# Kernel optimization log

Measured on AMD Instinct MI355X. Metric: run time of the kernel, lower is better.

Reference implementation:

```python
import jax, jax.numpy as jnp
import numpy as np

N_NODES = 100000
N_EDGES = 1600000
IN_F = 128
HID = 16
NEG_SLOPE = 0.2


def setup_inputs() -> dict:
    key = jax.random.key(0)
    ks = jax.random.split(key, 12)
    x = jax.random.normal(ks[0], (N_NODES, IN_F), dtype=jnp.float32)
    edge_index = jax.random.randint(ks[1], (2, N_EDGES), 0, N_NODES, dtype=jnp.int32)
    s1 = 1.0 / np.sqrt(IN_F)
    s2 = 1.0 / np.sqrt(2 * HID)
    # layer 1: heads=2, out=16, concat -> 32
    W1 = jax.random.normal(ks[2], (IN_F, 2 * HID), dtype=jnp.float32) * s1
    a_src1 = jax.random.normal(ks[3], (2, HID), dtype=jnp.float32) * s2
    a_dst1 = jax.random.normal(ks[4], (2, HID), dtype=jnp.float32) * s2
    b1 = jnp.zeros((2 * HID,), dtype=jnp.float32)
    # layer 2: heads=1, out=1
    W2 = jax.random.normal(ks[5], (2 * HID, 1), dtype=jnp.float32) * s2
    a_src2 = jax.random.normal(ks[6], (1, 1), dtype=jnp.float32)
    a_dst2 = jax.random.normal(ks[7], (1, 1), dtype=jnp.float32)
    b2 = jnp.zeros((1,), dtype=jnp.float32)
    return {"x": x, "edge_index": edge_index, "W1": W1, "a_src1": a_src1,
            "a_dst1": a_dst1, "b1": b1, "W2": W2, "a_src2": a_src2,
            "a_dst2": a_dst2, "b2": b2}


def gat_conv(x, src, dst, W, a_src, a_dst, bias, heads, out_ch, concat):
    # PyG GATConv: linear proj, per-edge leaky-relu score, segment softmax over
    # incoming edges (dst), scatter-add aggregation. Self loops already in src/dst.
    n = x.shape[0]
    h = (x @ W).reshape(n, heads, out_ch)                      # [N,H,C]
    alpha_s = (h * a_src[None]).sum(-1)                        # [N,H]
    alpha_d = (h * a_dst[None]).sum(-1)                        # [N,H]
    e = jax.nn.leaky_relu(alpha_s[src] + alpha_d[dst], NEG_SLOPE)  # [E,H]
    m = jax.lax.stop_gradient(jax.ops.segment_max(e, dst, num_segments=n))
    ex = jnp.exp(e - m[dst])
    denom = jax.ops.segment_sum(ex, dst, num_segments=n)       # [N,H]
    alpha = ex / (denom[dst] + 1e-16)                          # [E,H]
    out = jax.ops.segment_sum(alpha[..., None] * h[src], dst, num_segments=n)  # [N,H,C]
    out = out.reshape(n, heads * out_ch) if concat else out.mean(axis=1)
    return out + bias


def reference(x, edge_index, W1, a_src1, a_dst1, b1, W2, a_src2, a_dst2, b2):
    n = x.shape[0]
    loop = jnp.arange(n, dtype=edge_index.dtype)
    src = jnp.concatenate([edge_index[0], loop])
    dst = jnp.concatenate([edge_index[1], loop])
    h = jax.nn.elu(gat_conv(x, src, dst, W1, a_src1, a_dst1, b1, 2, HID, True))
    out = gat_conv(h, src, dst, W2, a_src2, a_dst2, b2, 1, 1, False)
    return out
```

## Files before the change

kernel.cpp:

```cpp
#include <hip/hip_runtime.h>
#include <math.h>

#define IN_F 128
#define C1 32
#define NEG 0.2f
#define BSZ 128
#define CAP 2560
#define EPB 2048
#define TPW 2

typedef _Float16 h16;
typedef _Float16 h16x2 __attribute__((ext_vector_type(2)));
typedef _Float16 h16x4 __attribute__((ext_vector_type(4)));
typedef _Float16 h16x8 __attribute__((ext_vector_type(8)));
typedef float f32x4 __attribute__((ext_vector_type(4)));

__device__ __forceinline__ float leaky(float x) { return x >= 0.f ? x : NEG * x; }

__global__ __launch_bounds__(256)
void k_fat(const float* __restrict__ x, const float* __restrict__ W1,
           const float* __restrict__ a_s, const float* __restrict__ a_d,
           h16* __restrict__ h1h, float* __restrict__ as1,
           float* __restrict__ ad1, int N,
           const int* __restrict__ ei, int E, int ET, int nbk,
           int* __restrict__ bcnt, int* __restrict__ ebuf, int nproj) {
    __shared__ int smem[6144];
    int t = threadIdx.x;
    if ((int)blockIdx.x < nproj) {
        int wid = t >> 6, lane = t & 63;
        int q = lane >> 4, r = lane & 15;
        h16x8 Bf[2][4];
        #pragma unroll
        for (int ct = 0; ct < 2; ++ct)
            #pragma unroll
            for (int kc = 0; kc < 4; ++kc)
                #pragma unroll
                for (int j = 0; j < 8; ++j)
                    Bf[ct][kc][j] = (h16)W1[(kc * 32 + q * 8 + j) * C1 + ct * 16 + r];
        float a_s0 = a_s[r], a_s1v = a_s[16 + r];
        float a_d0 = a_d[r], a_d1v = a_d[16 + r];
        #pragma unroll
        for (int tt = 0; tt < TPW; ++tt) {
            int tile = (blockIdx.x * 4 + wid) * TPW + tt;
            int m0 = tile << 4;
            if (m0 >= N) break;
            int row = m0 + r; if (row >= N) row = N - 1;
            const float* xr = x + (size_t)row * IN_F + q * 8;
            f32x4 acc0 = {0.f, 0.f, 0.f, 0.f};
            f32x4 acc1 = {0.f, 0.f, 0.f, 0.f};
            #pragma unroll
            for (int kc = 0; kc < 4; ++kc) {
                float4 xa = *(const float4*)(xr + kc * 32);
                float4 xb = *(const float4*)(xr + kc * 32 + 4);
                h16x8 A;
                A[0] = (h16)xa.x; A[1] = (h16)xa.y; A[2] = (h16)xa.z; A[3] = (h16)xa.w;
                A[4] = (h16)xb.x; A[5] = (h16)xb.y; A[6] = (h16)xb.z; A[7] = (h16)xb.w;
                acc0 = __builtin_amdgcn_mfma_f32_16x16x32_f16(A, Bf[0][kc], acc0, 0, 0, 0);
                acc1 = __builtin_amdgcn_mfma_f32_16x16x32_f16(A, Bf[1][kc], acc1, 0, 0, 0);
            }
            #pragma unroll
            for (int reg = 0; reg < 4; ++reg) {
                int node = m0 + q * 4 + reg;
                bool vld = node < N;
                float h0 = acc0[reg], h1 = acc1[reg];
                if (vld) {
                    h1h[(size_t)node * C1 + r]      = (h16)h0;
                    h1h[(size_t)node * C1 + 16 + r] = (h16)h1;
                }
                float s0 = h0 * a_s0, s1 = h1 * a_s1v;
                float d0 = h0 * a_d0, d1 = h1 * a_d1v;
                s0 += __shfl_xor(s0, 1); s0 += __shfl_xor(s0, 2); s0 += __shfl_xor(s0, 4); s0 += __shfl_xor(s0, 8);
                s1 += __shfl_xor(s1, 1); s1 += __shfl_xor(s1, 2); s1 += __shfl_xor(s1, 4); s1 += __shfl_xor(s1, 8);
                d0 += __shfl_xor(d0, 1); d0 += __shfl_xor(d0, 2); d0 += __shfl_xor(d0, 4); d0 += __shfl_xor(d0, 8);
                d1 += __shfl_xor(d1, 1); d1 += __shfl_xor(d1, 2); d1 += __shfl_xor(d1, 4); d1 += __shfl_xor(d1, 8);
                if (vld && r == 0) {
                    *(float2*)&as1[node * 2] = make_float2(s0, s1);
                    *(float2*)&ad1[node * 2] = make_float2(d0, d1);
                }
            }
        }
    } else {
        int* hist = smem;
        int* lcur = hist + 1024;
        int2* ecache = (int2*)(lcur + 1024);
        int bid = blockIdx.x - nproj;
        hist[t] = 0; hist[t + 256] = 0; hist[t + 512] = 0; hist[t + 768] = 0;
        __syncthreads();
        int i0 = bid * EPB, i1 = min(ET, i0 + EPB);
        for (int i = i0 + t; i < i1; i += 256) {
            int s, d;
            if (i < E) { s = ei[i]; d = ei[E + i]; } else { s = d = i - E; }
            ecache[i - i0] = make_int2(s, d);
            atomicAdd(&hist[d >> 7], 1);
        }
        __syncthreads();
        for (int b = t; b < nbk; b += 256) {
            int h = hist[b];
            int base = h ? atomicAdd(&bcnt[b], h) : 0;
            lcur[b] = b * CAP + base;
        }
        __syncthreads();
        for (int i = i0 + t; i < i1; i += 256) {
            int2 e = ecache[i - i0];
            int bkt = e.y >> 7;
            int pos = atomicAdd(&lcur[bkt], 1);
            if (pos < (bkt + 1) * CAP)
                ebuf[pos] = (e.x << 7) | (e.y & 127);
        }
    }
}

__global__ __launch_bounds__(512)
void k_bagg(const int* __restrict__ bcnt, const int* __restrict__ ebuf,
            int N, int nbk, int ET,
            const float* __restrict__ as1, const float* __restrict__ ad1,
            const float* __restrict__ b1, const float* __restrict__ W2,
            const h16* __restrict__ h1h, int* __restrict__ off,
            int* __restrict__ csr1, float* __restrict__ p2) {
    __shared__ int2 elist[CAP];
    __shared__ int deg[BSZ], sst[BSZ], cur[BSZ];
    __shared__ float adl[BSZ * 2];
    __shared__ int red[8];
    int b = blockIdx.x, t = threadIdx.x;
    int cnt = min(bcnt[b], CAP);
    int ebase = b * CAP;
    int n0 = b * BSZ;
    int part = 0;
    for (int k = t; k < b; k += 512) part += min(bcnt[k], CAP);
    part += __shfl_xor(part, 1);  part += __shfl_xor(part, 2);
    part += __shfl_xor(part, 4);  part += __shfl_xor(part, 8);
    part += __shfl_xor(part, 16); part += __shfl_xor(part, 32);
    if ((t & 63) == 0) red[t >> 6] = part;
    if (t < BSZ) {
        deg[t] = 0;
        int n = n0 + t;
        float2 v = (n < N) ? ((const float2*)ad1)[n] : make_float2(0.f, 0.f);
        adl[t * 2] = v.x; adl[t * 2 + 1] = v.y;
    }
    __syncthreads();
    int fbase = red[0] + red[1] + red[2] + red[3] + red[4] + red[5] + red[6] + red[7];
    if (b == nbk - 1 && t == 0) off[N] = ET;
    for (int i = t; i < cnt; i += 512)
        atomicAdd(&deg[ebuf[ebase + i] & 127], 1);
    __syncthreads();
    int v = (t < BSZ) ? deg[t] : 0;
    __syncthreads();
    for (int o = 1; o < BSZ; o <<= 1) {
        int xv = (t >= o && t < BSZ) ? deg[t - o] : 0;
        __syncthreads();
        if (t < BSZ) deg[t] += xv;
        __syncthreads();
    }
    if (t < BSZ) {
        int excl = deg[t] - v;
        sst[t] = excl; cur[t] = excl;
        if (n0 + t < N) off[n0 + t] = fbase + excl;
    }
    __syncthreads();
    for (int i = t; i < cnt; i += 512) {
        int e = ebuf[ebase + i];
        int dl = e & 127, s = e >> 7;
        float2 asv = ((const float2*)as1)[s];
        float w0 = __expf(leaky(asv.x + adl[dl * 2 + 0]));
        float w1 = __expf(leaky(asv.y + adl[dl * 2 + 1]));
        h16x2 wp = { (h16)w0, (h16)w1 };
        int p = atomicAdd(&cur[dl], 1);
        int2 rec; rec.x = s; rec.y = *(int*)&wp;
        elist[p] = rec;
        csr1[fbase + p] = s;
    }
    __syncthreads();
    int l = t & 7, slot = t >> 3, c0 = l * 4, head = l >> 2;
    float b1l[4] = { b1[c0], b1[c0 + 1], b1[c0 + 2], b1[c0 + 3] };
    float w2l[4] = { W2[c0], W2[c0 + 1], W2[c0 + 2], W2[c0 + 3] };
    #pragma unroll
    for (int pass = 0; pass < 2; ++pass) {
        int dl = pass * 64 + slot;
        int node = n0 + dl;
        if (node >= N) break;
        int j0 = sst[dl], j1 = deg[dl];
        float den = 0.f, a0 = 0.f, a1 = 0.f, a2 = 0.f, a3 = 0.f;
        for (int j = j0; j < j1; j += 4) {
            #pragma unroll
            for (int k = 0; k < 4; ++k) {
                int jj = j + k;
                bool valid = jj < j1;
                jj = valid ? jj : j0;
                int2 e = elist[jj];
                int s = e.x;
                h16x2 wv = *(h16x2*)&e.y;
                float w = valid ? (float)(head ? wv.y : wv.x) : 0.f;
                h16x4 hv = *(const h16x4*)(h1h + ((size_t)s << 5) + c0);
                den += w;
                a0 = fmaf(w, (float)hv.x, a0);
                a1 = fmaf(w, (float)hv.y, a1);
                a2 = fmaf(w, (float)hv.z, a2);
                a3 = fmaf(w, (float)hv.w, a3);
            }
        }
        float inv = 1.f / (den + 1e-16f);
        float o, val = 0.f;
        o = a0 * inv + b1l[0]; o = o > 0.f ? o : expm1f(o); val = fmaf(o, w2l[0], val);
        o = a1 * inv + b1l[1]; o = o > 0.f ? o : expm1f(o); val = fmaf(o, w2l[1], val);
        o = a2 * inv + b1l[2]; o = o > 0.f ? o : expm1f(o); val = fmaf(o, w2l[2], val);
        o = a3 * inv + b1l[3]; o = o > 0.f ? o : expm1f(o); val = fmaf(o, w2l[3], val);
        val += __shfl_xor(val, 1); val += __shfl_xor(val, 2); val += __shfl_xor(val, 4);
        if (l == 0) p2[node] = val;
    }
}

__global__ void k_l2(const int* __restrict__ off, const int* __restrict__ csr1,
                     const float* __restrict__ p2, const float* __restrict__ as2,
                     const float* __restrict__ ad2, const float* __restrict__ b2,
                     float* __restrict__ out, int N) {
    int i = blockIdx.x * blockDim.x + threadIdx.x;
    if (i >= N) return;
    float A = as2[0];
    float Bc = ad2[0] * p2[i];
    float den = 0.f, num = 0.f;
    int j0 = off[i], j1 = off[i + 1];
    for (int j = j0; j < j1; j += 4) {
        #pragma unroll
        for (int k = 0; k < 4; ++k) {
            int jj = j + k;
            bool valid = jj < j1;
            int s = csr1[valid ? jj : j0];
            float ps = p2[s];
            float w = valid ? __expf(leaky(fmaf(ps, A, Bc))) : 0.f;
            den += w;
            num = fmaf(w, ps, num);
        }
    }
    out[i] = num / (den + 1e-16f) + b2[0];
}

extern "C" void kernel_launch(void* const* d_in, const int* in_sizes, int n_in,
                              void* d_out, int out_size, void* d_ws, size_t ws_size,
                              hipStream_t stream) {
    const float* x    = (const float*)d_in[0];
    const int*   ei   = (const int*)d_in[1];
    const float* W1   = (const float*)d_in[2];
    const float* a_s1 = (const float*)d_in[3];
    const float* a_d1 = (const float*)d_in[4];
    const float* b1   = (const float*)d_in[5];
    const float* W2   = (const float*)d_in[6];
    const float* a_s2 = (const float*)d_in[7];
    const float* a_d2 = (const float*)d_in[8];
    const float* b2   = (const float*)d_in[9];
    float* out = (float*)d_out;

    const int N  = in_sizes[0] / IN_F;
    const int E  = in_sizes[1] / 2;
    const int ET = E + N;
    const int nbk = (N + BSZ - 1) / BSZ;

    float* w   = (float*)d_ws;
    float* as1 = w; w += (size_t)2 * N;
    float* ad1 = w; w += (size_t)2 * N;
    float* p2  = w; w += (size_t)N;
    h16* h1h   = (h16*)w;
    w += (size_t)16 * N;
    int* iw     = (int*)w;
    int* bcnt   = iw; iw += 1024;
    int* off    = iw; iw += (N + 1);
    int* csr1   = iw; iw += ET;
    int* ebuf   = iw; iw += (size_t)nbk * CAP;

    const int B = 256;
    const int ntile = (N + 15) / 16;
    const int nproj = (ntile + 4 * TPW - 1) / (4 * TPW);
    const int nblkA = (ET + EPB - 1) / EPB;

    hipMemsetAsync(bcnt, 0, 1024 * sizeof(int), stream);
    k_fat <<<nproj + nblkA, B, 0, stream>>>(x, W1, a_s1, a_d1, h1h, as1, ad1, N,
                                            ei, E, ET, nbk, bcnt, ebuf, nproj);
    k_bagg<<<nbk, 512, 0, stream>>>(bcnt, ebuf, N, nbk, ET, as1, ad1, b1, W2,
                                    h1h, off, csr1, p2);
    k_l2  <<<(N + B - 1) / B, B, 0, stream>>>(off, csr1, p2, a_s2, a_d2, b2, out, N);
}
```

Measured before the change: 181.9 us.

## Drop edge LDS cache, enlarge binning chunks, widen unroll, parallelize layer-2 per node

The binning phase no longer caches edges in shared memory. It re-reads edge_index from global memory in the scatter pass, which lets it use a much larger edges-per-block count (fewer blocks, fewer global bucket atomics) and a smaller LDS footprint. The layer-1 aggregation inner loop is unrolled to 8 instead of 4 for more memory-level parallelism. The layer-2 kernel now assigns 8 lanes per node with shuffle reductions instead of one thread per node, to spread uneven degree and gather latency across lanes. The cost is a second global read of the edges and fewer binning blocks, which may reduce parallelism in that phase.

```diff
diff --git a/kernel.cpp b/kernel.cpp
--- a/kernel.cpp
+++ b/kernel.cpp
@@ -6,7 +6,7 @@
 #define NEG 0.2f
 #define BSZ 128
 #define CAP 2560
-#define EPB 2048
+#define EPB 16384
 #define TPW 2
 
 typedef _Float16 h16;
@@ -24,7 +24,7 @@
            float* __restrict__ ad1, int N,
            const int* __restrict__ ei, int E, int ET, int nbk,
            int* __restrict__ bcnt, int* __restrict__ ebuf, int nproj) {
-    __shared__ int smem[6144];
+    __shared__ int smem[2048];
     int t = threadIdx.x;
     if ((int)blockIdx.x < nproj) {
         int wid = t >> 6, lane = t & 63;
@@ -81,16 +81,13 @@
         }
     } else {
         int* hist = smem;
-        int* lcur = hist + 1024;
-        int2* ecache = (int2*)(lcur + 1024);
+        int* lcur = smem + 1024;
         int bid = blockIdx.x - nproj;
         hist[t] = 0; hist[t + 256] = 0; hist[t + 512] = 0; hist[t + 768] = 0;
         __syncthreads();
         int i0 = bid * EPB, i1 = min(ET, i0 + EPB);
         for (int i = i0 + t; i < i1; i += 256) {
-            int s, d;
-            if (i < E) { s = ei[i]; d = ei[E + i]; } else { s = d = i - E; }
-            ecache[i - i0] = make_int2(s, d);
+            int d = (i < E) ? ei[E + i] : (i - E);
             atomicAdd(&hist[d >> 7], 1);
         }
         __syncthreads();
@@ -101,11 +98,12 @@
         }
         __syncthreads();
         for (int i = i0 + t; i < i1; i += 256) {
-            int2 e = ecache[i - i0];
-            int bkt = e.y >> 7;
+            int s, d;
+            if (i < E) { s = ei[i]; d = ei[E + i]; } else { s = d = i - E; }
+            int bkt = d >> 7;
             int pos = atomicAdd(&lcur[bkt], 1);
             if (pos < (bkt + 1) * CAP)
-                ebuf[pos] = (e.x << 7) | (e.y & 127);
+                ebuf[pos] = (s << 7) | (d & 127);
         }
     }
 }
@@ -180,9 +178,9 @@
         if (node >= N) break;
         int j0 = sst[dl], j1 = deg[dl];
         float den = 0.f, a0 = 0.f, a1 = 0.f, a2 = 0.f, a3 = 0.f;
-        for (int j = j0; j < j1; j += 4) {
-            #pragma unroll
-            for (int k = 0; k < 4; ++k) {
+        for (int j = j0; j < j1; j += 8) {
+            #pragma unroll
+            for (int k = 0; k < 8; ++k) {
                 int jj = j + k;
                 bool valid = jj < j1;
                 jj = valid ? jj : j0;
@@ -209,29 +207,27 @@
     }
 }
 
-__global__ void k_l2(const int* __restrict__ off, const int* __restrict__ csr1,
-                     const float* __restrict__ p2, const float* __restrict__ as2,
-                     const float* __restrict__ ad2, const float* __restrict__ b2,
-                     float* __restrict__ out, int N) {
-    int i = blockIdx.x * blockDim.x + threadIdx.x;
-    if (i >= N) return;
+__global__ __launch_bounds__(256)
+void k_l2(const int* __restrict__ off, const int* __restrict__ csr1,
+          const float* __restrict__ p2, const float* __restrict__ as2,
+          const float* __restrict__ ad2, const float* __restrict__ b2,
+          float* __restrict__ out, int N) {
+    int tid = blockIdx.x * 256 + threadIdx.x;
+    int g = tid >> 3, l = tid & 7;
+    if (g >= N) return;
     float A = as2[0];
-    float Bc = ad2[0] * p2[i];
+    float Bc = ad2[0] * p2[g];
     float den = 0.f, num = 0.f;
-    int j0 = off[i], j1 = off[i + 1];
-    for (int j = j0; j < j1; j += 4) {
-        #pragma unroll
-        for (int k = 0; k < 4; ++k) {
-            int jj = j + k;
-            bool valid = jj < j1;
-            int s = csr1[valid ? jj : j0];
-            float ps = p2[s];
-            float w = valid ? __expf(leaky(fmaf(ps, A, Bc))) : 0.f;
-            den += w;
-            num = fmaf(w, ps, num);
-        }
-    }
-    out[i] = num / (den + 1e-16f) + b2[0];
+    int j0 = off[g], j1 = off[g + 1];
+    for (int j = j0 + l; j < j1; j += 8) {
+        float ps = p2[csr1[j]];
+        float w = __expf(leaky(fmaf(ps, A, Bc)));
+        den += w;
+        num = fmaf(w, ps, num);
+    }
+    den += __shfl_xor(den, 1); den += __shfl_xor(den, 2); den += __shfl_xor(den, 4);
+    num += __shfl_xor(num, 1); num += __shfl_xor(num, 2); num += __shfl_xor(num, 4);
+    if (l == 0) out[g] = num / (den + 1e-16f) + b2[0];
 }
 
 extern "C" void kernel_launch(void* const* d_in, const int* in_sizes, int n_in,
@@ -276,5 +272,5 @@
                                             ei, E, ET, nbk, bcnt, ebuf, nproj);
     k_bagg<<<nbk, 512, 0, stream>>>(bcnt, ebuf, N, nbk, ET, as1, ad1, b1, W2,
                                     h1h, off, csr1, p2);
-    k_l2  <<<(N + B - 1) / B, B, 0, stream>>>(off, csr1, p2, a_s2, a_d2, b2, out, N);
-}
+    k_l2  <<<(N * 8 + B - 1) / B, B, 0, stream>>>(off, csr1, p2, a_s2, a_d2, b2, out, N);
+}
```

Result: slower. 210.0 us (+15.4%).
